# Kernel tuning notes

Measured on AMD Instinct MI355X. Metric: run time of the kernel, lower is better.

Reference implementation:

```python
import jax, jax.numpy as jnp
import numpy as np

N, E, G = 20000, 320000, 50
IN, H1, D1, H2, D2 = 64, 10, 64, 1, 128
NEG_SLOPE = 0.2  # DGL GATConv default


def _edge_softmax(e, dst, n):
    # segment softmax of per-edge scores e[E,H] grouped by destination node
    m = jax.ops.segment_max(e, dst, num_segments=n)
    m = jnp.where(jnp.isfinite(m), m, 0.0)  # nodes with zero in-degree
    ex = jnp.exp(e - m[dst])
    s = jax.ops.segment_sum(ex, dst, num_segments=n)
    return ex / jnp.where(s > 0, s, 1.0)[dst]


def _gat_layer(feat, W, al, ar, b, src, dst, n, h, d):
    ft = (feat @ W).reshape(n, h, d)              # [N,H,D]
    el = (ft * al).sum(-1)                        # [N,H]
    er = (ft * ar).sum(-1)                        # [N,H]
    e = jax.nn.leaky_relu(el[src] + er[dst], NEG_SLOPE)  # [E,H]
    a = _edge_softmax(e, dst, n)                  # [E,H]
    out = jax.ops.segment_sum(ft[src] * a[:, :, None], dst, num_segments=n)
    return out + b.reshape(1, h, d)


def setup_inputs() -> dict:
    key = jax.random.key(0)
    ks = jax.random.split(key, 16)
    feat = jax.random.normal(ks[0], (N, IN), dtype=jnp.float32)
    src = jax.random.randint(ks[1], (E,), 0, N)
    dst = jax.random.randint(ks[2], (E,), 0, N)
    graph_ids = jnp.sort(jax.random.randint(ks[3], (N,), 0, G))
    s1 = 1.0 / np.sqrt(IN)
    W1 = jax.random.normal(ks[4], (IN, H1 * D1), dtype=jnp.float32) * s1
    al1 = jax.random.normal(ks[5], (H1, D1), dtype=jnp.float32) * 0.1
    ar1 = jax.random.normal(ks[6], (H1, D1), dtype=jnp.float32) * 0.1
    b1 = jnp.zeros((H1 * D1,), dtype=jnp.float32)
    W2 = jax.random.normal(ks[7], (D1, H2 * D2), dtype=jnp.float32) * (1.0 / np.sqrt(D1))
    al2 = jax.random.normal(ks[8], (H2, D2), dtype=jnp.float32) * 0.1
    ar2 = jax.random.normal(ks[9], (H2, D2), dtype=jnp.float32) * 0.1
    b2 = jnp.zeros((H2 * D2,), dtype=jnp.float32)
    lw1 = jax.random.normal(ks[10], (D2, D2), dtype=jnp.float32) * (1.0 / np.sqrt(D2))
    lb1 = jnp.zeros((D2,), dtype=jnp.float32)
    lw2 = jax.random.normal(ks[11], (D2, 1), dtype=jnp.float32) * (1.0 / np.sqrt(D2))
    lb2 = jnp.zeros((1,), dtype=jnp.float32)
    return {"feat": feat, "src": src, "dst": dst, "graph_ids": graph_ids,
            "W1": W1, "al1": al1, "ar1": ar1, "b1": b1,
            "W2": W2, "al2": al2, "ar2": ar2, "b2": b2,
            "lw1": lw1, "lb1": lb1, "lw2": lw2, "lb2": lb2}


def reference(feat, src, dst, graph_ids, W1, al1, ar1, b1, W2, al2, ar2, b2, lw1, lb1, lw2, lb2):
    # eval mode: all dropouts are identity
    h = _gat_layer(feat, W1, al1, ar1, b1, src, dst, N, H1, D1)  # [N,10,64]
    h = jax.nn.relu(h)
    h = h.sum(axis=1)                                            # [N,64]
    h = _gat_layer(h, W2, al2, ar2, b2, src, dst, N, H2, D2)     # [N,1,128]
    h = jax.nn.relu(h)
    # readout_nodes op='max' over each graph in the batch
    r = jax.ops.segment_max(h, graph_ids, num_segments=G)        # [G,1,128]
    r = jnp.where(jnp.isfinite(r), r, 0.0)
    r = jax.nn.relu(r @ lw1 + lb1)
    r = jax.nn.relu(r @ lw2 + lb2)                               # [G,1,1]
    return r.reshape(-1)
```

## Files before the change

### kernel.cpp

```cpp
#include <hip/hip_runtime.h>
#include <hip/hip_fp16.h>

#define NN 20000
#define EE 320000
#define GG 50
#define IN_ 64
#define H1_ 10
#define D1_ 64
#define D2_ 128
#define F1 640
#define NEG 0.2f
#define CAP 128

static inline int cdiv(long long a, int b){ return (int)((a + b - 1) / b); }

typedef _Float16 half8 __attribute__((ext_vector_type(8)));
typedef float f32x4 __attribute__((ext_vector_type(4)));

__device__ inline float lrelu(float x){ return x > 0.f ? x : NEG * x; }

__device__ inline void fma_mix_lo(float& acc, float packed, float a){
  asm("v_fma_mix_f32 %0, %1, %2, %0 op_sel_hi:[1,0,0]"
      : "+v"(acc) : "v"(packed), "v"(a));
}
__device__ inline void fma_mix_hi(float& acc, float packed, float a){
  asm("v_fma_mix_f32 %0, %1, %2, %0 op_sel:[1,0,0] op_sel_hi:[1,0,0]"
      : "+v"(acc) : "v"(packed), "v"(a));
}

__global__ __launch_bounds__(256) void prep(
    const float* __restrict__ feat, const float* __restrict__ W1,
    _Float16* __restrict__ featH, _Float16* __restrict__ W1T,
    int* __restrict__ cur){
  int b = blockIdx.x, t = threadIdx.x;
  if(b < 1250){
    int idx = b * 1024 + t * 4;
    float4 v = *(const float4*)&feat[idx];
    _Float16 h4[4] = {(_Float16)v.x, (_Float16)v.y, (_Float16)v.z, (_Float16)v.w};
    *(float2*)&featH[idx] = *(float2*)h4;
    if(t < 16) cur[b * 16 + t] = 0;
  } else {
    int idx = (b - 1250) * 1024 + t * 4;
    int c = idx >> 6, k0 = idx & 63;
    _Float16 h4[4];
    #pragma unroll
    for(int j = 0; j < 4; j++) h4[j] = (_Float16)W1[(size_t)(k0 + j) * F1 + c];
    *(float2*)&W1T[idx] = *(float2*)h4;
  }
}

__global__ __launch_bounds__(256) void fused1(
    const int* __restrict__ src, const int* __restrict__ dst,
    int* __restrict__ cur, int* __restrict__ ssrc,
    const _Float16* __restrict__ featH, const _Float16* __restrict__ W1T,
    const float* __restrict__ al1, const float* __restrict__ ar1,
    _Float16* __restrict__ ft1h, float* __restrict__ elT, float* __restrict__ erT){
  __shared__ _Float16 sC[4][16][72];
  int b = blockIdx.x;
  if(b < 1250){
    int e = b * 256 + threadIdx.x;
    int d = dst[e];
    int pos = atomicAdd(&cur[d], 1);
    if(pos < CAP) ssrc[(d << 7) + pos] = src[e];
    return;
  }
  int b2 = b - 1250;
  int h = b2 % H1_;
  int n0 = (b2 / H1_) * 64;
  int tid = threadIdx.x, w = tid >> 6, l = tid & 63;
  int lr = l & 15, lk = l >> 4;
  int r0 = n0 + w * 16;
  int row = r0 + lr;
  half8 a0 = {}, a1 = {};
  if(row < NN){
    a0 = *(const half8*)&featH[row * 64 + lk * 8];
    a1 = *(const half8*)&featH[row * 64 + 32 + lk * 8];
  }
  f32x4 acc[4];
  #pragma unroll
  for(int c0 = 0; c0 < 4; c0++) acc[c0] = (f32x4){0.f, 0.f, 0.f, 0.f};
  #pragma unroll
  for(int c0 = 0; c0 < 4; c0++){
    int col = h * 64 + c0 * 16 + lr;
    half8 b0 = *(const half8*)&W1T[col * 64 + lk * 8];
    half8 b1 = *(const half8*)&W1T[col * 64 + 32 + lk * 8];
    acc[c0] = __builtin_amdgcn_mfma_f32_16x16x32_f16(a0, b0, acc[c0], 0, 0, 0);
    acc[c0] = __builtin_amdgcn_mfma_f32_16x16x32_f16(a1, b1, acc[c0], 0, 0, 0);
  }
  float elp[4] = {0.f,0.f,0.f,0.f}, erp[4] = {0.f,0.f,0.f,0.f};
  #pragma unroll
  for(int c0 = 0; c0 < 4; c0++){
    float al = al1[h * 64 + c0 * 16 + lr];
    float ar = ar1[h * 64 + c0 * 16 + lr];
    #pragma unroll
    for(int j = 0; j < 4; j++){
      elp[j] += acc[c0][j] * al;
      erp[j] += acc[c0][j] * ar;
    }
  }
  #pragma unroll
  for(int off = 1; off < 16; off <<= 1){
    #pragma unroll
    for(int j = 0; j < 4; j++){
      elp[j] += __shfl_xor(elp[j], off, 64);
      erp[j] += __shfl_xor(erp[j], off, 64);
    }
  }
  if(lr == 0){
    #pragma unroll
    for(int j = 0; j < 4; j++){
      int rj = r0 + lk * 4 + j;
      if(rj < NN){
        elT[(size_t)h * NN + rj] = elp[j];
        erT[(size_t)h * NN + rj] = erp[j];
      }
    }
  }
  #pragma unroll
  for(int c0 = 0; c0 < 4; c0++)
    #pragma unroll
    for(int j = 0; j < 4; j++)
      sC[w][lk * 4 + j][c0 * 16 + lr] = (_Float16)acc[c0][j];
  __syncthreads();
  #pragma unroll
  for(int it = 0; it < 2; it++){
    int idx = l + it * 64;
    int orow = idx >> 3, oc = (idx & 7) * 8;
    int grow = r0 + orow;
    if(grow < NN)
      *(float4*)&ft1h[((size_t)h * NN + grow) * 64 + oc] =
          *(const float4*)&sC[w][orow][oc];
  }
}

__global__ __launch_bounds__(256) void l1_head(
    const int* __restrict__ cur, const int* __restrict__ ssrc,
    const float* __restrict__ elT, const float* __restrict__ erT,
    const __half* __restrict__ ft1h, const float* __restrict__ b1,
    __half* __restrict__ out1h){
  __shared__ int2 pairs[4][2][2][32];
  int b = blockIdx.x;
  int xcd = b & 7, slot = b >> 3;
  int h, blk;
  if(slot < 1250){ h = xcd; blk = slot; }
  else {
    int s = slot - 1250; h = 8 + (xcd >> 2); blk = (xcd & 3) * 313 + s;
    if(blk >= 1250) return;
  }
  int wave = threadIdx.x >> 6, lane = threadIdx.x & 63;
  int half = lane >> 5, l32 = lane & 31;
  int eg = l32 >> 4, dg = l32 & 15;
  int dnA = blk * 16 + wave * 4 + half * 2;
  int dnB = dnA + 1;
  int degA = min(cur[dnA], CAP), degB = min(cur[dnB], CAP);
  int baseA = dnA << 7, baseB = dnB << 7;
  float4 accA = make_float4(0.f,0.f,0.f,0.f);
  float4 accB = make_float4(0.f,0.f,0.f,0.f);
  const char* fbase = (const char*)(ft1h + (size_t)h * NN * 64) + (dg << 3);
  const float* elh = elT + (size_t)h * NN;
  float erA = erT[(size_t)h * NN + dnA];
  float erB = erT[(size_t)h * NN + dnB];
  int2* wpA = pairs[wave][half][0];
  int2* wpB = pairs[wave][half][1];

  if(__any(degA > 32 || degB > 32)){
    #pragma unroll
    for(int which = 0; which < 2; which++){
      int base = which ? baseB : baseA;
      int deg  = which ? degB : degA;
      float er_h = which ? erB : erA;
      float4* accp = which ? &accB : &accA;
      int2* wp = which ? wpB : wpA;
      float sm = 0.f;
      for(int i = l32; i < deg; i += 32)
        sm += __expf(lrelu(elh[ssrc[base + i]] + er_h));
      #pragma unroll
      for(int o = 1; o < 32; o <<= 1) sm += __shfl_xor(sm, o, 64);
      float inv = deg > 0 ? 1.f / sm : 0.f;
      for(int c = 0; c < deg; c += 32){
        int m = deg - c; if(m > 32) m = 32;
        if(l32 < m){
          int sn = ssrc[base + c + l32];
          wp[l32] = make_int2(__float_as_int(__expf(lrelu(elh[sn] + er_h)) * inv), sn << 7);
        }
        for(int i = eg; i < m; i += 2){
          int2 pr = wp[i];
          float a_i = __int_as_float(pr.x);
          float2 raw = *(const float2*)(fbase + pr.y);
          fma_mix_lo(accp->x, raw.x, a_i); fma_mix_hi(accp->y, raw.x, a_i);
          fma_mix_lo(accp->z, raw.y, a_i); fma_mix_hi(accp->w, raw.y, a_i);
        }
      }
    }
  } else {
    int snA = 0, snB = 0;
    if(l32 < degA) snA = ssrc[baseA + l32];
    if(l32 < degB) snB = ssrc[baseB + l32];
    float pA = 0.f, pB = 0.f;
    if(l32 < degA) pA = __expf(lrelu(elh[snA] + erA));
    if(l32 < degB) pB = __expf(lrelu(elh[snB] + erB));
    float smA = pA, smB = pB;
    #pragma unroll
    for(int o = 1; o < 32; o <<= 1){
      smA += __shfl_xor(smA, o, 64);
      smB += __shfl_xor(smB, o, 64);
    }
    float invA = degA > 0 ? 1.f / smA : 0.f;
    float invB = degB > 0 ? 1.f / smB : 0.f;
    wpA[l32] = l32 < degA ? make_int2(__float_as_int(pA * invA), snA << 7)
                          : make_int2(0, 0);
    wpB[l32] = l32 < degB ? make_int2(__float_as_int(pB * invB), snB << 7)
                          : make_int2(0, 0);
    int maxd = max(degA, degB);
    int i = eg;
    for(; i + 2 < maxd; i += 4){
      int2 a0 = wpA[i], a1 = wpA[i + 2];
      int2 b0 = wpB[i], b1 = wpB[i + 2];
      float2 ra0 = *(const float2*)(fbase + a0.y);
      float2 rb0 = *(const float2*)(fbase + b0.y);
      float2 ra1 = *(const float2*)(fbase + a1.y);
      float2 rb1 = *(const float2*)(fbase + b1.y);
      float aa0 = __int_as_float(a0.x), aa1 = __int_as_float(a1.x);
      float ab0 = __int_as_float(b0.x), ab1 = __int_as_float(b1.x);
      fma_mix_lo(accA.x, ra0.x, aa0); fma_mix_hi(accA.y, ra0.x, aa0);
      fma_mix_lo(accA.z, ra0.y, aa0); fma_mix_hi(accA.w, ra0.y, aa0);
      fma_mix_lo(accB.x, rb0.x, ab0); fma_mix_hi(accB.y, rb0.x, ab0);
      fma_mix_lo(accB.z, rb0.y, ab0); fma_mix_hi(accB.w, rb0.y, ab0);
      fma_mix_lo(accA.x, ra1.x, aa1); fma_mix_hi(accA.y, ra1.x, aa1);
      fma_mix_lo(accA.z, ra1.y, aa1); fma_mix_hi(accA.w, ra1.y, aa1);
      fma_mix_lo(accB.x, rb1.x, ab1); fma_mix_hi(accB.y, rb1.x, ab1);
      fma_mix_lo(accB.z, rb1.y, ab1); fma_mix_hi(accB.w, rb1.y, ab1);
    }
    if(i < maxd){
      int2 a0 = wpA[i], b0 = wpB[i];
      float2 ra0 = *(const float2*)(fbase + a0.y);
      float2 rb0 = *(const float2*)(fbase + b0.y);
      float aa0 = __int_as_float(a0.x), ab0 = __int_as_float(b0.x);
      fma_mix_lo(accA.x, ra0.x, aa0); fma_mix_hi(accA.y, ra0.x, aa0);
      fma_mix_lo(accA.z, ra0.y, aa0); fma_mix_hi(accA.w, ra0.y, aa0);
      fma_mix_lo(accB.x, rb0.x, ab0); fma_mix_hi(accB.y, rb0.x, ab0);
      fma_mix_lo(accB.z, rb0.y, ab0); fma_mix_hi(accB.w, rb0.y, ab0);
    }
  }
  accA.x += __shfl_xor(accA.x, 16, 64); accB.x += __shfl_xor(accB.x, 16, 64);
  accA.y += __shfl_xor(accA.y, 16, 64); accB.y += __shfl_xor(accB.y, 16, 64);
  accA.z += __shfl_xor(accA.z, 16, 64); accB.z += __shfl_xor(accB.z, 16, 64);
  accA.w += __shfl_xor(accA.w, 16, 64); accB.w += __shfl_xor(accB.w, 16, 64);
  if(eg == 0){
    int d = dg << 2;
    const float* bp = &b1[h * 64 + d];
    float b0 = bp[0], b1v = bp[1], b2v = bp[2], b3 = bp[3];
    union { __half2 h2[2]; float2 f2; } u;
    u.h2[0] = __floats2half2_rn(fmaxf(accA.x + b0, 0.f), fmaxf(accA.y + b1v, 0.f));
    u.h2[1] = __floats2half2_rn(fmaxf(accA.z + b2v, 0.f), fmaxf(accA.w + b3, 0.f));
    *(float2*)&out1h[(size_t)dnA * F1 + h * 64 + d] = u.f2;
    u.h2[0] = __floats2half2_rn(fmaxf(accB.x + b0, 0.f), fmaxf(accB.y + b1v, 0.f));
    u.h2[1] = __floats2half2_rn(fmaxf(accB.z + b2v, 0.f), fmaxf(accB.w + b3, 0.f));
    *(float2*)&out1h[(size_t)dnB * F1 + h * 64 + d] = u.f2;
  }
}

__global__ __launch_bounds__(256) void gemm2(
    const __half* __restrict__ out1h, const float* __restrict__ W2,
    const float* __restrict__ al2, const float* __restrict__ ar2,
    __half* __restrict__ ft2h, float* __restrict__ el, float* __restrict__ er){
  __shared__ float AsT[64][36];
  __shared__ __half Bsh[64][132];
  int n0 = blockIdx.x * 32;
  int tid = threadIdx.x;
  #pragma unroll
  for(int l = 0; l < 2; l++){
    int idx = tid + l * 256;
    int r = idx >> 4, c4 = (idx & 15) << 2;
    float4 sv = make_float4(0.f,0.f,0.f,0.f);
    if(n0 + r < NN){
      const __half* rp = &out1h[(size_t)(n0 + r) * F1 + c4];
      #pragma unroll
      for(int hh = 0; hh < H1_; hh++){
        float2 raw = *(const float2*)(rp + hh * 64);
        const __half2* hp = (const __half2*)&raw;
        float2 f0 = __half22float2(hp[0]);
        float2 f1 = __half22float2(hp[1]);
        sv.x += f0.x; sv.y += f0.y; sv.z += f1.x; sv.w += f1.y;
      }
    }
    AsT[c4+0][r] = sv.x; AsT[c4+1][r] = sv.y; AsT[c4+2][r] = sv.z; AsT[c4+3][r] = sv.w;
  }
  #pragma unroll
  for(int l = 0; l < 8; l++){
    int idx = tid + l * 256;
    int k = idx >> 5, c4 = (idx & 31) << 2;
    float4 w = *(const float4*)&W2[(size_t)k * D2_ + c4];
    union { __half2 h2[2]; float2 f2; } u;
    u.h2[0] = __floats2half2_rn(w.x, w.y);
    u.h2[1] = __floats2half2_rn(w.z, w.w);
    *(float2*)&Bsh[k][c4] = u.f2;
  }
  __syncthreads();
  int tr = tid >> 5, tc = tid & 31;
  float acc[4][4];
  #pragma unroll
  for(int i = 0; i < 4; i++)
    #pragma unroll
    for(int j = 0; j < 4; j++) acc[i][j] = 0.f;
  #pragma unroll 8
  for(int k = 0; k < 64; k++){
    float4 a4 = *(const float4*)&AsT[k][tr << 2];
    float2 b2v = *(const float2*)&Bsh[k][tc << 2];
    float av[4] = {a4.x, a4.y, a4.z, a4.w};
    #pragma unroll
    for(int i = 0; i < 4; i++){
      fma_mix_lo(acc[i][0], b2v.x, av[i]);
      fma_mix_hi(acc[i][1], b2v.x, av[i]);
      fma_mix_lo(acc[i][2], b2v.y, av[i]);
      fma_mix_hi(acc[i][3], b2v.y, av[i]);
    }
  }
  float al4[4], ar4[4];
  #pragma unroll
  for(int j = 0; j < 4; j++){
    al4[j] = al2[(tc << 2) + j];
    ar4[j] = ar2[(tc << 2) + j];
  }
  int col = tc << 2;
  int half = col >> 6, c64 = col & 63;
  #pragma unroll
  for(int i = 0; i < 4; i++){
    int row = n0 + (tr << 2) + i;
    bool ok = row < NN;
    if(ok){
      union { __half2 h2[2]; float2 f2; } u;
      u.h2[0] = __floats2half2_rn(acc[i][0], acc[i][1]);
      u.h2[1] = __floats2half2_rn(acc[i][2], acc[i][3]);
      *(float2*)&ft2h[((size_t)half * NN + row) * 64 + c64] = u.f2;
    }
    float e1 = acc[i][0]*al4[0] + acc[i][1]*al4[1] + acc[i][2]*al4[2] + acc[i][3]*al4[3];
    float e2 = acc[i][0]*ar4[0] + acc[i][1]*ar4[1] + acc[i][2]*ar4[2] + acc[i][3]*ar4[3];
    #pragma unroll
    for(int off = 1; off < 32; off <<= 1){
      e1 += __shfl_xor(e1, off, 64);
      e2 += __shfl_xor(e2, off, 64);
    }
    if(tc == 0 && ok){ el[row] = e1; er[row] = e2; }
  }
}

__global__ __launch_bounds__(256) void l2_head(
    const int* __restrict__ cur, const int* __restrict__ ssrc,
    const float* __restrict__ el, const float* __restrict__ er,
    const __half* __restrict__ ft2h, const float* __restrict__ b2,
    float* __restrict__ h2v){
  __shared__ int2 pairs[4][2][2][32];
  int b = blockIdx.x;
  int xcd = b & 7, slot = b >> 3;
  int halfd = xcd >> 2;
  int blk = (xcd & 3) * 313 + slot;
  if(blk >= 1250) return;
  int wave = threadIdx.x >> 6, lane = threadIdx.x & 63;
  int half = lane >> 5, l32 = lane & 31;
  int eg = l32 >> 4, dg = l32 & 15;
  int dnA = blk * 16 + wave * 4 + half * 2;
  int dnB = dnA + 1;
  int degA = min(cur[dnA], CAP), degB = min(cur[dnB], CAP);
  int baseA = dnA << 7, baseB = dnB << 7;
  float4 accA = make_float4(0.f,0.f,0.f,0.f);
  float4 accB = make_float4(0.f,0.f,0.f,0.f);
  const char* fbase = (const char*)(ft2h + (size_t)halfd * NN * 64) + (dg << 3);
  float erA = er[dnA], erB = er[dnB];
  int2* wpA = pairs[wave][half][0];
  int2* wpB = pairs[wave][half][1];

  if(__any(degA > 32 || degB > 32)){
    #pragma unroll
    for(int which = 0; which < 2; which++){
      int base = which ? baseB : baseA;
      int deg  = which ? degB : degA;
      float er_d = which ? erB : erA;
      float4* accp = which ? &accB : &accA;
      int2* wp = which ? wpB : wpA;
      float sm = 0.f;
      for(int i = l32; i < deg; i += 32)
        sm += __expf(lrelu(el[ssrc[base + i]] + er_d));
      #pragma unroll
      for(int o = 1; o < 32; o <<= 1) sm += __shfl_xor(sm, o, 64);
      float inv = deg > 0 ? 1.f / sm : 0.f;
      for(int c = 0; c < deg; c += 32){
        int m = deg - c; if(m > 32) m = 32;
        if(l32 < m){
          int sn = ssrc[base + c + l32];
          wp[l32] = make_int2(__float_as_int(__expf(lrelu(el[sn] + er_d)) * inv), sn << 7);
        }
        for(int i = eg; i < m; i += 2){
          int2 pr = wp[i];
          float a_i = __int_as_float(pr.x);
          float2 raw = *(const float2*)(fbase + pr.y);
          fma_mix_lo(accp->x, raw.x, a_i); fma_mix_hi(accp->y, raw.x, a_i);
          fma_mix_lo(accp->z, raw.y, a_i); fma_mix_hi(accp->w, raw.y, a_i);
        }
      }
    }
  } else {
    int snA = 0, snB = 0;
    if(l32 < degA) snA = ssrc[baseA + l32];
    if(l32 < degB) snB = ssrc[baseB + l32];
    float pA = 0.f, pB = 0.f;
    if(l32 < degA) pA = __expf(lrelu(el[snA] + erA));
    if(l32 < degB) pB = __expf(lrelu(el[snB] + erB));
    float smA = pA, smB = pB;
    #pragma unroll
    for(int o = 1; o < 32; o <<= 1){
      smA += __shfl_xor(smA, o, 64);
      smB += __shfl_xor(smB, o, 64);
    }
    float invA = degA > 0 ? 1.f / smA : 0.f;
    float invB = degB > 0 ? 1.f / smB : 0.f;
    wpA[l32] = l32 < degA ? make_int2(__float_as_int(pA * invA), snA << 7)
                          : make_int2(0, 0);
    wpB[l32] = l32 < degB ? make_int2(__float_as_int(pB * invB), snB << 7)
                          : make_int2(0, 0);
    int maxd = max(degA, degB);
    int i = eg;
    for(; i + 2 < maxd; i += 4){
      int2 a0 = wpA[i], a1 = wpA[i + 2];
      int2 b0 = wpB[i], b1 = wpB[i + 2];
      float2 ra0 = *(const float2*)(fbase + a0.y);
      float2 rb0 = *(const float2*)(fbase + b0.y);
      float2 ra1 = *(const float2*)(fbase + a1.y);
      float2 rb1 = *(const float2*)(fbase + b1.y);
      float aa0 = __int_as_float(a0.x), aa1 = __int_as_float(a1.x);
      float ab0 = __int_as_float(b0.x), ab1 = __int_as_float(b1.x);
      fma_mix_lo(accA.x, ra0.x, aa0); fma_mix_hi(accA.y, ra0.x, aa0);
      fma_mix_lo(accA.z, ra0.y, aa0); fma_mix_hi(accA.w, ra0.y, aa0);
      fma_mix_lo(accB.x, rb0.x, ab0); fma_mix_hi(accB.y, rb0.x, ab0);
      fma_mix_lo(accB.z, rb0.y, ab0); fma_mix_hi(accB.w, rb0.y, ab0);
      fma_mix_lo(accA.x, ra1.x, aa1); fma_mix_hi(accA.y, ra1.x, aa1);
      fma_mix_lo(accA.z, ra1.y, aa1); fma_mix_hi(accA.w, ra1.y, aa1);
      fma_mix_lo(accB.x, rb1.x, ab1); fma_mix_hi(accB.y, rb1.x, ab1);
      fma_mix_lo(accB.z, rb1.y, ab1); fma_mix_hi(accB.w, rb1.y, ab1);
    }
    if(i < maxd){
      int2 a0 = wpA[i], b0 = wpB[i];
      float2 ra0 = *(const float2*)(fbase + a0.y);
      float2 rb0 = *(const float2*)(fbase + b0.y);
      float aa0 = __int_as_float(a0.x), ab0 = __int_as_float(b0.x);
      fma_mix_lo(accA.x, ra0.x, aa0); fma_mix_hi(accA.y, ra0.x, aa0);
      fma_mix_lo(accA.z, ra0.y, aa0); fma_mix_hi(accA.w, ra0.y, aa0);
      fma_mix_lo(accB.x, rb0.x, ab0); fma_mix_hi(accB.y, rb0.x, ab0);
      fma_mix_lo(accB.z, rb0.y, ab0); fma_mix_hi(accB.w, rb0.y, ab0);
    }
  }
  accA.x += __shfl_xor(accA.x, 16, 64); accB.x += __shfl_xor(accB.x, 16, 64);
  accA.y += __shfl_xor(accA.y, 16, 64); accB.y += __shfl_xor(accB.y, 16, 64);
  accA.z += __shfl_xor(accA.z, 16, 64); accB.z += __shfl_xor(accB.z, 16, 64);
  accA.w += __shfl_xor(accA.w, 16, 64); accB.w += __shfl_xor(accB.w, 16, 64);
  if(eg == 0){
    int doff = halfd * 64 + (dg << 2);
    const float* bp = &b2[doff];
    float b0 = bp[0], b1v = bp[1], b2v = bp[2], b3 = bp[3];
    float4 o;
    o.x = fmaxf(accA.x + b0, 0.f);
    o.y = fmaxf(accA.y + b1v, 0.f);
    o.z = fmaxf(accA.z + b2v, 0.f);
    o.w = fmaxf(accA.w + b3, 0.f);
    *(float4*)&h2v[(size_t)dnA * D2_ + doff] = o;
    o.x = fmaxf(accB.x + b0, 0.f);
    o.y = fmaxf(accB.y + b1v, 0.f);
    o.z = fmaxf(accB.z + b2v, 0.f);
    o.w = fmaxf(accB.w + b3, 0.f);
    *(float4*)&h2v[(size_t)dnB * D2_ + doff] = o;
  }
}

__global__ __launch_bounds__(256) void readout(
    const float* __restrict__ h2v, const int* __restrict__ gid,
    const float* __restrict__ lw1, const float* __restrict__ lb1,
    const float* __restrict__ lw2, const float* __restrict__ lb2,
    float* __restrict__ out){
  __shared__ int sb[2];
  __shared__ float mx2[2][D2_];
  __shared__ float rv[D2_];
  __shared__ float t[D2_];
  int g = blockIdx.x, tid = threadIdx.x;
  int d = tid & 127, hh = tid >> 7;
  if(tid < 2){
    int tgt = g + tid;
    int lo = 0, hi = NN;
    while(lo < hi){ int mid = (lo + hi) >> 1; if(gid[mid] < tgt) lo = mid + 1; else hi = mid; }
    sb[tid] = lo;
  }
  __syncthreads();
  int gs = sb[0], ge = sb[1];
  float m0 = 0.f, m1 = 0.f, m2 = 0.f, m3 = 0.f;
  int n = gs + hh;
  for(; n + 6 < ge; n += 8){
    m0 = fmaxf(m0, h2v[(size_t)(n + 0) * D2_ + d]);
    m1 = fmaxf(m1, h2v[(size_t)(n + 2) * D2_ + d]);
    m2 = fmaxf(m2, h2v[(size_t)(n + 4) * D2_ + d]);
    m3 = fmaxf(m3, h2v[(size_t)(n + 6) * D2_ + d]);
  }
  for(; n < ge; n += 2) m0 = fmaxf(m0, h2v[(size_t)n * D2_ + d]);
  mx2[hh][d] = fmaxf(fmaxf(m0, m1), fmaxf(m2, m3));
  __syncthreads();
  if(tid < D2_) rv[d] = fmaxf(mx2[0][d], mx2[1][d]);
  __syncthreads();
  if(tid < D2_){
    float acc = lb1[d];
    #pragma unroll 8
    for(int k = 0; k < D2_; k++) acc += rv[k] * lw1[k * D2_ + d];
    acc = acc > 0.f ? acc : 0.f;
    t[d] = acc * lw2[d];
  }
  __syncthreads();
  for(int off = 64; off > 0; off >>= 1){
    if(tid < off) t[tid] += t[tid + off];
    __syncthreads();
  }
  if(tid == 0){
    float v = t[0] + lb2[0];
    out[g] = v > 0.f ? v : 0.f;
  }
}

extern "C" void kernel_launch(void* const* d_in, const int* in_sizes, int n_in,
                              void* d_out, int out_size, void* d_ws, size_t ws_size,
                              hipStream_t stream) {
  const float* feat = (const float*)d_in[0];
  const int*   src  = (const int*)d_in[1];
  const int*   dst  = (const int*)d_in[2];
  const int*   gid  = (const int*)d_in[3];
  const float* W1   = (const float*)d_in[4];
  const float* al1  = (const float*)d_in[5];
  const float* ar1  = (const float*)d_in[6];
  const float* b1   = (const float*)d_in[7];
  const float* W2   = (const float*)d_in[8];
  const float* al2  = (const float*)d_in[9];
  const float* ar2  = (const float*)d_in[10];
  const float* b2   = (const float*)d_in[11];
  const float* lw1  = (const float*)d_in[12];
  const float* lb1  = (const float*)d_in[13];
  const float* lw2  = (const float*)d_in[14];
  const float* lb2  = (const float*)d_in[15];
  float* out = (float*)d_out;

  float* ws = (float*)d_ws;
  size_t o = 0;
  _Float16* ft1h = (_Float16*)(ws + o); o += (size_t)NN * F1 / 2;
  __half* out1h = (__half*)(ws + o); o += (size_t)NN * F1 / 2;
  __half* ft2h = (__half*)(ws + o); o += (size_t)NN * D2_ / 2;
  float* h2v  = ws + o; o += (size_t)NN * D2_;
  float* el1  = ws + o; o += (size_t)NN * H1_;
  float* er1  = ws + o; o += (size_t)NN * H1_;
  float* el2  = ws + o; o += NN;
  float* er2  = ws + o; o += NN;
  int* cur    = (int*)(ws + o); o += NN;
  int* ssrc   = (int*)(ws + o); o += (size_t)NN * CAP;
  _Float16* featH = (_Float16*)(ws + o); o += (size_t)NN * IN_ / 2;
  _Float16* W1T   = (_Float16*)(ws + o); o += (size_t)F1 * IN_ / 2;

  prep<<<1290, 256, 0, stream>>>(feat, W1, featH, W1T, cur);
  fused1<<<1250 + H1_ * cdiv(NN, 64), 256, 0, stream>>>(
      src, dst, cur, ssrc, featH, W1T, al1, ar1, ft1h, el1, er1);
  l1_head<<<8 * (1250 + 313), 256, 0, stream>>>(cur, ssrc, el1, er1,
                                                (const __half*)ft1h, b1, out1h);
  gemm2<<<cdiv(NN, 32), 256, 0, stream>>>(out1h, W2, al2, ar2, ft2h, el2, er2);
  l2_head<<<8 * 313, 256, 0, stream>>>(cur, ssrc, el2, er2, ft2h, b2, h2v);
  readout<<<GG, 256, 0, stream>>>(h2v, gid, lw1, lb1, lw2, lb2, out);
}
```

Measured before the change: 149.0 us.

## Use MFMA for layer-2 GEMM and widen aggregation gathers to 16 bytes

Rewrites gemm2 to use 16x16x32 f16 MFMA instructions, with W2 pre-transposed to half precision in the prep kernel, 64 rows per block, and the head-sum done in half8 vector adds. It also changes both aggregation kernels so each lane gathers 16-byte chunks (8 halfs) across 4 edge groups instead of 8-byte chunks across 2. The goal is to cut GEMM ALU cost and the number of gather instructions. Summing the 10 heads in fp16 lowers accumulation precision compared with the previous fp32 sum.

```diff
diff --git a/kernel.cpp b/kernel.cpp
--- a/kernel.cpp
+++ b/kernel.cpp
@@ -27,10 +27,17 @@
   asm("v_fma_mix_f32 %0, %1, %2, %0 op_sel:[1,0,0] op_sel_hi:[1,0,0]"
       : "+v"(acc) : "v"(packed), "v"(a));
 }
+__device__ inline void fma8(float4& c0, float4& c1, const float4& r, float a){
+  fma_mix_lo(c0.x, r.x, a); fma_mix_hi(c0.y, r.x, a);
+  fma_mix_lo(c0.z, r.y, a); fma_mix_hi(c0.w, r.y, a);
+  fma_mix_lo(c1.x, r.z, a); fma_mix_hi(c1.y, r.z, a);
+  fma_mix_lo(c1.z, r.w, a); fma_mix_hi(c1.w, r.w, a);
+}
 
 __global__ __launch_bounds__(256) void prep(
     const float* __restrict__ feat, const float* __restrict__ W1,
-    _Float16* __restrict__ featH, _Float16* __restrict__ W1T,
+    const float* __restrict__ W2, _Float16* __restrict__ featH,
+    _Float16* __restrict__ W1T, _Float16* __restrict__ W2T,
     int* __restrict__ cur){
   int b = blockIdx.x, t = threadIdx.x;
   if(b < 1250){
@@ -39,13 +46,20 @@
     _Float16 h4[4] = {(_Float16)v.x, (_Float16)v.y, (_Float16)v.z, (_Float16)v.w};
     *(float2*)&featH[idx] = *(float2*)h4;
     if(t < 16) cur[b * 16 + t] = 0;
-  } else {
+  } else if(b < 1290){
     int idx = (b - 1250) * 1024 + t * 4;
     int c = idx >> 6, k0 = idx & 63;
     _Float16 h4[4];
     #pragma unroll
     for(int j = 0; j < 4; j++) h4[j] = (_Float16)W1[(size_t)(k0 + j) * F1 + c];
     *(float2*)&W1T[idx] = *(float2*)h4;
+  } else {
+    int idx = (b - 1290) * 1024 + t * 4;
+    int c = idx >> 6, k0 = idx & 63;
+    _Float16 h4[4];
+    #pragma unroll
+    for(int j = 0; j < 4; j++) h4[j] = (_Float16)W2[(size_t)(k0 + j) * D2_ + c];
+    *(float2*)&W2T[idx] = *(float2*)h4;
   }
 }
 
@@ -149,14 +163,14 @@
   }
   int wave = threadIdx.x >> 6, lane = threadIdx.x & 63;
   int half = lane >> 5, l32 = lane & 31;
-  int eg = l32 >> 4, dg = l32 & 15;
+  int eg = l32 >> 3, dg = l32 & 7;
   int dnA = blk * 16 + wave * 4 + half * 2;
   int dnB = dnA + 1;
   int degA = min(cur[dnA], CAP), degB = min(cur[dnB], CAP);
   int baseA = dnA << 7, baseB = dnB << 7;
-  float4 accA = make_float4(0.f,0.f,0.f,0.f);
-  float4 accB = make_float4(0.f,0.f,0.f,0.f);
-  const char* fbase = (const char*)(ft1h + (size_t)h * NN * 64) + (dg << 3);
+  float4 accA0 = make_float4(0.f,0.f,0.f,0.f), accA1 = accA0;
+  float4 accB0 = accA0, accB1 = accA0;
+  const char* fbase = (const char*)(ft1h + (size_t)h * NN * 64) + (dg << 4);
   const float* elh = elT + (size_t)h * NN;
   float erA = erT[(size_t)h * NN + dnA];
   float erB = erT[(size_t)h * NN + dnB];
@@ -169,7 +183,8 @@
       int base = which ? baseB : baseA;
       int deg  = which ? degB : degA;
       float er_h = which ? erB : erA;
-      float4* accp = which ? &accB : &accA;
+      float4* p0 = which ? &accB0 : &accA0;
+      float4* p1 = which ? &accB1 : &accA1;
       int2* wp = which ? wpB : wpA;
       float sm = 0.f;
       for(int i = l32; i < deg; i += 32)
@@ -183,12 +198,10 @@
           int sn = ssrc[base + c + l32];
           wp[l32] = make_int2(__float_as_int(__expf(lrelu(elh[sn] + er_h)) * inv), sn << 7);
         }
-        for(int i = eg; i < m; i += 2){
+        for(int i = eg; i < m; i += 4){
           int2 pr = wp[i];
-          float a_i = __int_as_float(pr.x);
-          float2 raw = *(const float2*)(fbase + pr.y);
-          fma_mix_lo(accp->x, raw.x, a_i); fma_mix_hi(accp->y, raw.x, a_i);
-          fma_mix_lo(accp->z, raw.y, a_i); fma_mix_hi(accp->w, raw.y, a_i);
+          float4 raw = *(const float4*)(fbase + pr.y);
+          fma8(*p0, *p1, raw, __int_as_float(pr.x));
         }
       }
     }
@@ -213,135 +226,127 @@
                           : make_int2(0, 0);
     int maxd = max(degA, degB);
     int i = eg;
-    for(; i + 2 < maxd; i += 4){
-      int2 a0 = wpA[i], a1 = wpA[i + 2];
-      int2 b0 = wpB[i], b1 = wpB[i + 2];
-      float2 ra0 = *(const float2*)(fbase + a0.y);
-      float2 rb0 = *(const float2*)(fbase + b0.y);
-      float2 ra1 = *(const float2*)(fbase + a1.y);
-      float2 rb1 = *(const float2*)(fbase + b1.y);
-      float aa0 = __int_as_float(a0.x), aa1 = __int_as_float(a1.x);
-      float ab0 = __int_as_float(b0.x), ab1 = __int_as_float(b1.x);
-      fma_mix_lo(accA.x, ra0.x, aa0); fma_mix_hi(accA.y, ra0.x, aa0);
-      fma_mix_lo(accA.z, ra0.y, aa0); fma_mix_hi(accA.w, ra0.y, aa0);
-      fma_mix_lo(accB.x, rb0.x, ab0); fma_mix_hi(accB.y, rb0.x, ab0);
-      fma_mix_lo(accB.z, rb0.y, ab0); fma_mix_hi(accB.w, rb0.y, ab0);
-      fma_mix_lo(accA.x, ra1.x, aa1); fma_mix_hi(accA.y, ra1.x, aa1);
-      fma_mix_lo(accA.z, ra1.y, aa1); fma_mix_hi(accA.w, ra1.y, aa1);
-      fma_mix_lo(accB.x, rb1.x, ab1); fma_mix_hi(accB.y, rb1.x, ab1);
-      fma_mix_lo(accB.z, rb1.y, ab1); fma_mix_hi(accB.w, rb1.y, ab1);
+    for(; i + 4 < maxd; i += 8){
+      int2 a0 = wpA[i], a1 = wpA[i + 4];
+      int2 b0 = wpB[i], b1 = wpB[i + 4];
+      float4 ra0 = *(const float4*)(fbase + a0.y);
+      float4 rb0 = *(const float4*)(fbase + b0.y);
+      float4 ra1 = *(const float4*)(fbase + a1.y);
+      float4 rb1 = *(const float4*)(fbase + b1.y);
+      fma8(accA0, accA1, ra0, __int_as_float(a0.x));
+      fma8(accB0, accB1, rb0, __int_as_float(b0.x));
+      fma8(accA0, accA1, ra1, __int_as_float(a1.x));
+      fma8(accB0, accB1, rb1, __int_as_float(b1.x));
     }
     if(i < maxd){
       int2 a0 = wpA[i], b0 = wpB[i];
-      float2 ra0 = *(const float2*)(fbase + a0.y);
-      float2 rb0 = *(const float2*)(fbase + b0.y);
-      float aa0 = __int_as_float(a0.x), ab0 = __int_as_float(b0.x);
-      fma_mix_lo(accA.x, ra0.x, aa0); fma_mix_hi(accA.y, ra0.x, aa0);
-      fma_mix_lo(accA.z, ra0.y, aa0); fma_mix_hi(accA.w, ra0.y, aa0);
-      fma_mix_lo(accB.x, rb0.x, ab0); fma_mix_hi(accB.y, rb0.x, ab0);
-      fma_mix_lo(accB.z, rb0.y, ab0); fma_mix_hi(accB.w, rb0.y, ab0);
-    }
-  }
-  accA.x += __shfl_xor(accA.x, 16, 64); accB.x += __shfl_xor(accB.x, 16, 64);
-  accA.y += __shfl_xor(accA.y, 16, 64); accB.y += __shfl_xor(accB.y, 16, 64);
-  accA.z += __shfl_xor(accA.z, 16, 64); accB.z += __shfl_xor(accB.z, 16, 64);
-  accA.w += __shfl_xor(accA.w, 16, 64); accB.w += __shfl_xor(accB.w, 16, 64);
+      float4 ra0 = *(const float4*)(fbase + a0.y);
+      float4 rb0 = *(const float4*)(fbase + b0.y);
+      fma8(accA0, accA1, ra0, __int_as_float(a0.x));
+      fma8(accB0, accB1, rb0, __int_as_float(b0.x));
+    }
+  }
+  #pragma unroll
+  for(int off = 8; off <= 16; off <<= 1){
+    accA0.x += __shfl_xor(accA0.x, off, 64); accA0.y += __shfl_xor(accA0.y, off, 64);
+    accA0.z += __shfl_xor(accA0.z, off, 64); accA0.w += __shfl_xor(accA0.w, off, 64);
+    accA1.x += __shfl_xor(accA1.x, off, 64); accA1.y += __shfl_xor(accA1.y, off, 64);
+    accA1.z += __shfl_xor(accA1.z, off, 64); accA1.w += __shfl_xor(accA1.w, off, 64);
+    accB0.x += __shfl_xor(accB0.x, off, 64); accB0.y += __shfl_xor(accB0.y, off, 64);
+    accB0.z += __shfl_xor(accB0.z, off, 64); accB0.w += __shfl_xor(accB0.w, off, 64);
+    accB1.x += __shfl_xor(accB1.x, off, 64); accB1.y += __shfl_xor(accB1.y, off, 64);
+    accB1.z += __shfl_xor(accB1.z, off, 64); accB1.w += __shfl_xor(accB1.w, off, 64);
+  }
   if(eg == 0){
-    int d = dg << 2;
+    int d = dg << 3;
     const float* bp = &b1[h * 64 + d];
-    float b0 = bp[0], b1v = bp[1], b2v = bp[2], b3 = bp[3];
-    union { __half2 h2[2]; float2 f2; } u;
-    u.h2[0] = __floats2half2_rn(fmaxf(accA.x + b0, 0.f), fmaxf(accA.y + b1v, 0.f));
-    u.h2[1] = __floats2half2_rn(fmaxf(accA.z + b2v, 0.f), fmaxf(accA.w + b3, 0.f));
-    *(float2*)&out1h[(size_t)dnA * F1 + h * 64 + d] = u.f2;
-    u.h2[0] = __floats2half2_rn(fmaxf(accB.x + b0, 0.f), fmaxf(accB.y + b1v, 0.f));
-    u.h2[1] = __floats2half2_rn(fmaxf(accB.z + b2v, 0.f), fmaxf(accB.w + b3, 0.f));
-    *(float2*)&out1h[(size_t)dnB * F1 + h * 64 + d] = u.f2;
+    union { __half2 h2[4]; float4 f4; } u;
+    u.h2[0] = __floats2half2_rn(fmaxf(accA0.x + bp[0], 0.f), fmaxf(accA0.y + bp[1], 0.f));
+    u.h2[1] = __floats2half2_rn(fmaxf(accA0.z + bp[2], 0.f), fmaxf(accA0.w + bp[3], 0.f));
+    u.h2[2] = __floats2half2_rn(fmaxf(accA1.x + bp[4], 0.f), fmaxf(accA1.y + bp[5], 0.f));
+    u.h2[3] = __floats2half2_rn(fmaxf(accA1.z + bp[6], 0.f), fmaxf(accA1.w + bp[7], 0.f));
+    *(float4*)&out1h[(size_t)dnA * F1 + h * 64 + d] = u.f4;
+    u.h2[0] = __floats2half2_rn(fmaxf(accB0.x + bp[0], 0.f), fmaxf(accB0.y + bp[1], 0.f));
+    u.h2[1] = __floats2half2_rn(fmaxf(accB0.z + bp[2], 0.f), fmaxf(accB0.w + bp[3], 0.f));
+    u.h2[2] = __floats2half2_rn(fmaxf(accB1.x + bp[4], 0.f), fmaxf(accB1.y + bp[5], 0.f));
+    u.h2[3] = __floats2half2_rn(fmaxf(accB1.z + bp[6], 0.f), fmaxf(accB1.w + bp[7], 0.f));
+    *(float4*)&out1h[(size_t)dnB * F1 + h * 64 + d] = u.f4;
   }
 }
 
 __global__ __launch_bounds__(256) void gemm2(
-    const __half* __restrict__ out1h, const float* __restrict__ W2,
+    const _Float16* __restrict__ out1h, const _Float16* __restrict__ W2T,
     const float* __restrict__ al2, const float* __restrict__ ar2,
-    __half* __restrict__ ft2h, float* __restrict__ el, float* __restrict__ er){
-  __shared__ float AsT[64][36];
-  __shared__ __half Bsh[64][132];
-  int n0 = blockIdx.x * 32;
-  int tid = threadIdx.x;
-  #pragma unroll
-  for(int l = 0; l < 2; l++){
-    int idx = tid + l * 256;
-    int r = idx >> 4, c4 = (idx & 15) << 2;
-    float4 sv = make_float4(0.f,0.f,0.f,0.f);
-    if(n0 + r < NN){
-      const __half* rp = &out1h[(size_t)(n0 + r) * F1 + c4];
-      #pragma unroll
-      for(int hh = 0; hh < H1_; hh++){
-        float2 raw = *(const float2*)(rp + hh * 64);
-        const __half2* hp = (const __half2*)&raw;
-        float2 f0 = __half22float2(hp[0]);
-        float2 f1 = __half22float2(hp[1]);
-        sv.x += f0.x; sv.y += f0.y; sv.z += f1.x; sv.w += f1.y;
-      }
-    }
-    AsT[c4+0][r] = sv.x; AsT[c4+1][r] = sv.y; AsT[c4+2][r] = sv.z; AsT[c4+3][r] = sv.w;
-  }
-  #pragma unroll
-  for(int l = 0; l < 8; l++){
-    int idx = tid + l * 256;
-    int k = idx >> 5, c4 = (idx & 31) << 2;
-    float4 w = *(const float4*)&W2[(size_t)k * D2_ + c4];
-    union { __half2 h2[2]; float2 f2; } u;
-    u.h2[0] = __floats2half2_rn(w.x, w.y);
-    u.h2[1] = __floats2half2_rn(w.z, w.w);
-    *(float2*)&Bsh[k][c4] = u.f2;
-  }
+    _Float16* __restrict__ ft2h, float* __restrict__ el, float* __restrict__ er){
+  __shared__ _Float16 sC[4][16][136];
+  int n0 = blockIdx.x * 64;
+  int tid = threadIdx.x, w = tid >> 6, l = tid & 63;
+  int lr = l & 15, lk = l >> 4;
+  int r0 = n0 + w * 16;
+  int row = r0 + lr;
+  half8 a0 = {}, a1 = {};
+  if(row < NN){
+    const _Float16* rp = out1h + (size_t)row * F1;
+    half8 s0 = *(const half8*)(rp + lk * 8);
+    half8 s1 = *(const half8*)(rp + 32 + lk * 8);
+    #pragma unroll
+    for(int hh = 1; hh < H1_; hh++){
+      s0 += *(const half8*)(rp + hh * 64 + lk * 8);
+      s1 += *(const half8*)(rp + hh * 64 + 32 + lk * 8);
+    }
+    a0 = s0; a1 = s1;
+  }
+  f32x4 acc[8];
+  #pragma unroll
+  for(int c0 = 0; c0 < 8; c0++) acc[c0] = (f32x4){0.f, 0.f, 0.f, 0.f};
+  #pragma unroll
+  for(int c0 = 0; c0 < 8; c0++){
+    int col = c0 * 16 + lr;
+    half8 b0 = *(const half8*)&W2T[col * 64 + lk * 8];
+    half8 b1 = *(const half8*)&W2T[col * 64 + 32 + lk * 8];
+    acc[c0] = __builtin_amdgcn_mfma_f32_16x16x32_f16(a0, b0, acc[c0], 0, 0, 0);
+    acc[c0] = __builtin_amdgcn_mfma_f32_16x16x32_f16(a1, b1, acc[c0], 0, 0, 0);
+  }
+  float elp[4] = {0.f,0.f,0.f,0.f}, erp[4] = {0.f,0.f,0.f,0.f};
+  #pragma unroll
+  for(int c0 = 0; c0 < 8; c0++){
+    float al = al2[c0 * 16 + lr];
+    float ar = ar2[c0 * 16 + lr];
+    #pragma unroll
+    for(int j = 0; j < 4; j++){
+      elp[j] += acc[c0][j] * al;
+      erp[j] += acc[c0][j] * ar;
+    }
+  }
+  #pragma unroll
+  for(int off = 1; off < 16; off <<= 1){
+    #pragma unroll
+    for(int j = 0; j < 4; j++){
+      elp[j] += __shfl_xor(elp[j], off, 64);
+      erp[j] += __shfl_xor(erp[j], off, 64);
+    }
+  }
+  if(lr == 0){
+    #pragma unroll
+    for(int j = 0; j < 4; j++){
+      int rj = r0 + lk * 4 + j;
+      if(rj < NN){ el[rj] = elp[j]; er[rj] = erp[j]; }
+    }
+  }
+  #pragma unroll
+  for(int c0 = 0; c0 < 8; c0++)
+    #pragma unroll
+    for(int j = 0; j < 4; j++)
+      sC[w][lk * 4 + j][c0 * 16 + lr] = (_Float16)acc[c0][j];
   __syncthreads();
-  int tr = tid >> 5, tc = tid & 31;
-  float acc[4][4];
-  #pragma unroll
-  for(int i = 0; i < 4; i++)
-    #pragma unroll
-    for(int j = 0; j < 4; j++) acc[i][j] = 0.f;
-  #pragma unroll 8
-  for(int k = 0; k < 64; k++){
-    float4 a4 = *(const float4*)&AsT[k][tr << 2];
-    float2 b2v = *(const float2*)&Bsh[k][tc << 2];
-    float av[4] = {a4.x, a4.y, a4.z, a4.w};
-    #pragma unroll
-    for(int i = 0; i < 4; i++){
-      fma_mix_lo(acc[i][0], b2v.x, av[i]);
-      fma_mix_hi(acc[i][1], b2v.x, av[i]);
-      fma_mix_lo(acc[i][2], b2v.y, av[i]);
-      fma_mix_hi(acc[i][3], b2v.y, av[i]);
-    }
-  }
-  float al4[4], ar4[4];
-  #pragma unroll
-  for(int j = 0; j < 4; j++){
-    al4[j] = al2[(tc << 2) + j];
-    ar4[j] = ar2[(tc << 2) + j];
-  }
-  int col = tc << 2;
-  int half = col >> 6, c64 = col & 63;
-  #pragma unroll
-  for(int i = 0; i < 4; i++){
-    int row = n0 + (tr << 2) + i;
-    bool ok = row < NN;
-    if(ok){
-      union { __half2 h2[2]; float2 f2; } u;
-      u.h2[0] = __floats2half2_rn(acc[i][0], acc[i][1]);
-      u.h2[1] = __floats2half2_rn(acc[i][2], acc[i][3]);
-      *(float2*)&ft2h[((size_t)half * NN + row) * 64 + c64] = u.f2;
-    }
-    float e1 = acc[i][0]*al4[0] + acc[i][1]*al4[1] + acc[i][2]*al4[2] + acc[i][3]*al4[3];
-    float e2 = acc[i][0]*ar4[0] + acc[i][1]*ar4[1] + acc[i][2]*ar4[2] + acc[i][3]*ar4[3];
-    #pragma unroll
-    for(int off = 1; off < 32; off <<= 1){
-      e1 += __shfl_xor(e1, off, 64);
-      e2 += __shfl_xor(e2, off, 64);
-    }
-    if(tc == 0 && ok){ el[row] = e1; er[row] = e2; }
+  #pragma unroll
+  for(int it = 0; it < 4; it++){
+    int idx = l + it * 64;
+    int orow = idx >> 4, oc = (idx & 15) * 8;
+    int grow = r0 + orow;
+    if(grow < NN)
+      *(float4*)&ft2h[((size_t)(oc >> 6) * NN + grow) * 64 + (oc & 63)] =
+          *(const float4*)&sC[w][orow][oc];
   }
 }
 
@@ -358,14 +363,14 @@
   if(blk >= 1250) return;
   int wave = threadIdx.x >> 6, lane = threadIdx.x & 63;
   int half = lane >> 5, l32 = lane & 31;
-  int eg = l32 >> 4, dg = l32 & 15;
+  int eg = l32 >> 3, dg = l32 & 7;
   int dnA = blk * 16 + wave * 4 + half * 2;
   int dnB = dnA + 1;
   int degA = min(cur[dnA], CAP), degB = min(cur[dnB], CAP);
   int baseA = dnA << 7, baseB = dnB << 7;
-  float4 accA = make_float4(0.f,0.f,0.f,0.f);
-  float4 accB = make_float4(0.f,0.f,0.f,0.f);
-  const char* fbase = (const char*)(ft2h + (size_t)halfd * NN * 64) + (dg << 3);
+  float4 accA0 = make_float4(0.f,0.f,0.f,0.f), accA1 = accA0;
+  float4 accB0 = accA0, accB1 = accA0;
+  const char* fbase = (const char*)(ft2h + (size_t)halfd * NN * 64) + (dg << 4);
   float erA = er[dnA], erB = er[dnB];
   int2* wpA = pairs[wave][half][0];
   int2* wpB = pairs[wave][half][1];
@@ -376,7 +381,8 @@
       int base = which ? baseB : baseA;
       int deg  = which ? degB : degA;
       float er_d = which ? erB : erA;
-      float4* accp = which ? &accB : &accA;
+      float4* p0 = which ? &accB0 : &accA0;
+      float4* p1 = which ? &accB1 : &accA1;
       int2* wp = which ? wpB : wpA;
       float sm = 0.f;
       for(int i = l32; i < deg; i += 32)
@@ -390,12 +396,10 @@
           int sn = ssrc[base + c + l32];
           wp[l32] = make_int2(__float_as_int(__expf(lrelu(el[sn] + er_d)) * inv), sn << 7);
         }
-        for(int i = eg; i < m; i += 2){
+        for(int i = eg; i < m; i += 4){
           int2 pr = wp[i];
-          float a_i = __int_as_float(pr.x);
-          float2 raw = *(const float2*)(fbase + pr.y);
-          fma_mix_lo(accp->x, raw.x, a_i); fma_mix_hi(accp->y, raw.x, a_i);
-          fma_mix_lo(accp->z, raw.y, a_i); fma_mix_hi(accp->w, raw.y, a_i);
+          float4 raw = *(const float4*)(fbase + pr.y);
+          fma8(*p0, *p1, raw, __int_as_float(pr.x));
         }
       }
     }
@@ -420,54 +424,61 @@
                           : make_int2(0, 0);
     int maxd = max(degA, degB);
     int i = eg;
-    for(; i + 2 < maxd; i += 4){
-      int2 a0 = wpA[i], a1 = wpA[i + 2];
-      int2 b0 = wpB[i], b1 = wpB[i + 2];
-      float2 ra0 = *(const float2*)(fbase + a0.y);
-      float2 rb0 = *(const float2*)(fbase + b0.y);
-      float2 ra1 = *(const float2*)(fbase + a1.y);
-      float2 rb1 = *(const float2*)(fbase + b1.y);
-      float aa0 = __int_as_float(a0.x), aa1 = __int_as_float(a1.x);
-      float ab0 = __int_as_float(b0.x), ab1 = __int_as_float(b1.x);
-      fma_mix_lo(accA.x, ra0.x, aa0); fma_mix_hi(accA.y, ra0.x, aa0);
-      fma_mix_lo(accA.z, ra0.y, aa0); fma_mix_hi(accA.w, ra0.y, aa0);
-      fma_mix_lo(accB.x, rb0.x, ab0); fma_mix_hi(accB.y, rb0.x, ab0);
-      fma_mix_lo(accB.z, rb0.y, ab0); fma_mix_hi(accB.w, rb0.y, ab0);
-      fma_mix_lo(accA.x, ra1.x, aa1); fma_mix_hi(accA.y, ra1.x, aa1);
-      fma_mix_lo(accA.z, ra1.y, aa1); fma_mix_hi(accA.w, ra1.y, aa1);
-      fma_mix_lo(accB.x, rb1.x, ab1); fma_mix_hi(accB.y, rb1.x, ab1);
-      fma_mix_lo(accB.z, rb1.y, ab1); fma_mix_hi(accB.w, rb1.y, ab1);
+    for(; i + 4 < maxd; i += 8){
+      int2 a0 = wpA[i], a1 = wpA[i + 4];
+      int2 b0 = wpB[i], b1 = wpB[i + 4];
+      float4 ra0 = *(const float4*)(fbase + a0.y);
+      float4 rb0 = *(const float4*)(fbase + b0.y);
+      float4 ra1 = *(const float4*)(fbase + a1.y);
+      float4 rb1 = *(const float4*)(fbase + b1.y);
+      fma8(accA0, accA1, ra0, __int_as_float(a0.x));
+      fma8(accB0, accB1, rb0, __int_as_float(b0.x));
+      fma8(accA0, accA1, ra1, __int_as_float(a1.x));
+      fma8(accB0, accB1, rb1, __int_as_float(b1.x));
     }
     if(i < maxd){
       int2 a0 = wpA[i], b0 = wpB[i];
-      float2 ra0 = *(const float2*)(fbase + a0.y);
-      float2 rb0 = *(const float2*)(fbase + b0.y);
-      float aa0 = __int_as_float(a0.x), ab0 = __int_as_float(b0.x);
-      fma_mix_lo(accA.x, ra0.x, aa0); fma_mix_hi(accA.y, ra0.x, aa0);
-      fma_mix_lo(accA.z, ra0.y, aa0); fma_mix_hi(accA.w, ra0.y, aa0);
-      fma_mix_lo(accB.x, rb0.x, ab0); fma_mix_hi(accB.y, rb0.x, ab0);
-      fma_mix_lo(accB.z, rb0.y, ab0); fma_mix_hi(accB.w, rb0.y, ab0);
-    }
-  }
-  accA.x += __shfl_xor(accA.x, 16, 64); accB.x += __shfl_xor(accB.x, 16, 64);
-  accA.y += __shfl_xor(accA.y, 16, 64); accB.y += __shfl_xor(accB.y, 16, 64);
-  accA.z += __shfl_xor(accA.z, 16, 64); accB.z += __shfl_xor(accB.z, 16, 64);
-  accA.w += __shfl_xor(accA.w, 16, 64); accB.w += __shfl_xor(accB.w, 16, 64);
+      float4 ra0 = *(const float4*)(fbase + a0.y);
+      float4 rb0 = *(const float4*)(fbase + b0.y);
+      fma8(accA0, accA1, ra0, __int_as_float(a0.x));
+      fma8(accB0, accB1, rb0, __int_as_float(b0.x));
+    }
+  }
+  #pragma unroll
+  for(int off = 8; off <= 16; off <<= 1){
+    accA0.x += __shfl_xor(accA0.x, off, 64); accA0.y += __shfl_xor(accA0.y, off, 64);
+    accA0.z += __shfl_xor(accA0.z, off, 64); accA0.w += __shfl_xor(accA0.w, off, 64);
+    accA1.x += __shfl_xor(accA1.x, off, 64); accA1.y += __shfl_xor(accA1.y, off, 64);
+    accA1.z += __shfl_xor(accA1.z, off, 64); accA1.w += __shfl_xor(accA1.w, off, 64);
+    accB0.x += __shfl_xor(accB0.x, off, 64); accB0.y += __shfl_xor(accB0.y, off, 64);
+    accB0.z += __shfl_xor(accB0.z, off, 64); accB0.w += __shfl_xor(accB0.w, off, 64);
+    accB1.x += __shfl_xor(accB1.x, off, 64); accB1.y += __shfl_xor(accB1.y, off, 64);
+    accB1.z += __shfl_xor(accB1.z, off, 64); accB1.w += __shfl_xor(accB1.w, off, 64);
+  }
   if(eg == 0){
-    int doff = halfd * 64 + (dg << 2);
+    int doff = halfd * 64 + (dg << 3);
     const float* bp = &b2[doff];
-    float b0 = bp[0], b1v = bp[1], b2v = bp[2], b3 = bp[3];
     float4 o;
-    o.x = fmaxf(accA.x + b0, 0.f);
-    o.y = fmaxf(accA.y + b1v, 0.f);
-    o.z = fmaxf(accA.z + b2v, 0.f);
-    o.w = fmaxf(accA.w + b3, 0.f);
+    o.x = fmaxf(accA0.x + bp[0], 0.f);
+    o.y = fmaxf(accA0.y + bp[1], 0.f);
+    o.z = fmaxf(accA0.z + bp[2], 0.f);
+    o.w = fmaxf(accA0.w + bp[3], 0.f);
     *(float4*)&h2v[(size_t)dnA * D2_ + doff] = o;
-    o.x = fmaxf(accB.x + b0, 0.f);
-    o.y = fmaxf(accB.y + b1v, 0.f);
-    o.z = fmaxf(accB.z + b2v, 0.f);
-    o.w = fmaxf(accB.w + b3, 0.f);
+    o.x = fmaxf(accA1.x + bp[4], 0.f);
+    o.y = fmaxf(accA1.y + bp[5], 0.f);
+    o.z = fmaxf(accA1.z + bp[6], 0.f);
+    o.w = fmaxf(accA1.w + bp[7], 0.f);
+    *(float4*)&h2v[(size_t)dnA * D2_ + doff + 4] = o;
+    o.x = fmaxf(accB0.x + bp[0], 0.f);
+    o.y = fmaxf(accB0.y + bp[1], 0.f);
+    o.z = fmaxf(accB0.z + bp[2], 0.f);
+    o.w = fmaxf(accB0.w + bp[3], 0.f);
     *(float4*)&h2v[(size_t)dnB * D2_ + doff] = o;
+    o.x = fmaxf(accB1.x + bp[4], 0.f);
+    o.y = fmaxf(accB1.y + bp[5], 0.f);
+    o.z = fmaxf(accB1.z + bp[6], 0.f);
+    o.w = fmaxf(accB1.w + bp[7], 0.f);
+    *(float4*)&h2v[(size_t)dnB * D2_ + doff + 4] = o;
   }
 }
 
@@ -545,8 +556,8 @@
   float* ws = (float*)d_ws;
   size_t o = 0;
   _Float16* ft1h = (_Float16*)(ws + o); o += (size_t)NN * F1 / 2;
-  __half* out1h = (__half*)(ws + o); o += (size_t)NN * F1 / 2;
-  __half* ft2h = (__half*)(ws + o); o += (size_t)NN * D2_ / 2;
+  _Float16* out1h = (_Float16*)(ws + o); o += (size_t)NN * F1 / 2;
+  _Float16* ft2h = (_Float16*)(ws + o); o += (size_t)NN * D2_ / 2;
   float* h2v  = ws + o; o += (size_t)NN * D2_;
   float* el1  = ws + o; o += (size_t)NN * H1_;
   float* er1  = ws + o; o += (size_t)NN * H1_;
@@ -556,13 +567,16 @@
   int* ssrc   = (int*)(ws + o); o += (size_t)NN * CAP;
   _Float16* featH = (_Float16*)(ws + o); o += (size_t)NN * IN_ / 2;
   _Float16* W1T   = (_Float16*)(ws + o); o += (size_t)F1 * IN_ / 2;
-
-  prep<<<1290, 256, 0, stream>>>(feat, W1, featH, W1T, cur);
+  _Float16* W2T   = (_Float16*)(ws + o); o += (size_t)D2_ * IN_ / 2;
+
+  prep<<<1298, 256, 0, stream>>>(feat, W1, W2, featH, W1T, W2T, cur);
   fused1<<<1250 + H1_ * cdiv(NN, 64), 256, 0, stream>>>(
       src, dst, cur, ssrc, featH, W1T, al1, ar1, ft1h, el1, er1);
   l1_head<<<8 * (1250 + 313), 256, 0, stream>>>(cur, ssrc, el1, er1,
-                                                (const __half*)ft1h, b1, out1h);
-  gemm2<<<cdiv(NN, 32), 256, 0, stream>>>(out1h, W2, al2, ar2, ft2h, el2, er2);
-  l2_head<<<8 * 313, 256, 0, stream>>>(cur, ssrc, el2, er2, ft2h, b2, h2v);
+                                                (const __half*)ft1h, b1,
+                                                (__half*)out1h);
+  gemm2<<<cdiv(NN, 64), 256, 0, stream>>>(out1h, W2T, al2, ar2, ft2h, el2, er2);
+  l2_head<<<8 * 313, 256, 0, stream>>>(cur, ssrc, el2, er2,
+                                       (const __half*)ft2h, b2, h2v);
   readout<<<GG, 256, 0, stream>>>(h2v, gid, lw1, lb1, lw2, lb2, out);
 }
```

Result: faster. 136.3 us (-8.5%).
